# Kernel tuning notes

Measured on AMD Instinct MI355X. Metric: run time of the kernel, lower is better.

Reference implementation:

```python
import jax, jax.numpy as jnp
import numpy as np

MODEL_DIM = 1024
TOTAL_DIM = 1024
N_HEADS = 16
HEAD_DIM = TOTAL_DIM // N_HEADS


def setup_inputs() -> dict:
    key = jax.random.key(0)
    k1, k2, k3 = jax.random.split(key, 3)
    query = jax.random.normal(k1, (2, 2048, MODEL_DIM), dtype=jnp.float32)
    # nn.Linear(model_dim, 3*total_dim, bias=False): store as [in, out] for x @ W
    W_in = jax.random.normal(k2, (MODEL_DIM, 3 * TOTAL_DIM), dtype=jnp.float32) / np.sqrt(MODEL_DIM)
    W_out = jax.random.normal(k3, (TOTAL_DIM, MODEL_DIM), dtype=jnp.float32) / np.sqrt(TOTAL_DIM)
    return {"query": query, "W_in": W_in, "W_out": W_out}


def reference(query, W_in, W_out):
    B, S, _ = query.shape
    qkv = query @ W_in                      # [B, S, 3*D]
    q, k, v = jnp.split(qkv, 3, axis=-1)    # each [B, S, D]

    def to_heads(t):
        return t.reshape(B, S, N_HEADS, HEAD_DIM).transpose(0, 2, 1, 3)  # [B,H,S,d]

    q, k, v = to_heads(q), to_heads(k), to_heads(v)
    scale = 1.0 / np.sqrt(HEAD_DIM).astype(np.float32)
    scores = jnp.einsum('bhqd,bhkd->bhqk', q, k) * scale  # [B,H,S,S]
    causal = jnp.tril(jnp.ones((S, S), dtype=bool))
    scores = jnp.where(causal, scores, jnp.finfo(scores.dtype).min)
    probs = jax.nn.softmax(scores, axis=-1)
    attn = jnp.einsum('bhqk,bhkd->bhqd', probs, v)        # [B,H,S,d]
    attn = attn.transpose(0, 2, 1, 3).reshape(B, S, TOTAL_DIM)
    return attn @ W_out                     # [B, S, model_dim]
```

## Files before the change

### kernel.cpp

```cpp
#include <hip/hip_runtime.h>


typedef __bf16 bf16x8 __attribute__((ext_vector_type(8)));
typedef __bf16 bf16x4 __attribute__((ext_vector_type(4)));
typedef short s16x4 __attribute__((ext_vector_type(4)));
typedef float f32x4 __attribute__((ext_vector_type(4)));
typedef int i32x2 __attribute__((ext_vector_type(2)));

#define B_   2
#define S_   2048
#define DM   1024
#define NH   16
#define HD   64
#define N3   3072
#define M_   4096

#define SCALE_LOG2E 0.180336884f

__device__ __forceinline__ unsigned short f2bf(float f) {
  unsigned int u = __float_as_uint(f);
  u += 0x7fffu + ((u >> 16) & 1u);
  return (unsigned short)(u >> 16);
}

__device__ __forceinline__ void gload_lds16(void* lds, const void* g) {
  __builtin_amdgcn_global_load_lds(
      (__attribute__((address_space(1))) void*)g,
      (__attribute__((address_space(3))) void*)lds, 16, 0, 0);
}

__device__ __forceinline__ f32x4 mfma16(bf16x4 a, bf16x4 b, f32x4 c) {
#if __has_builtin(__builtin_amdgcn_mfma_f32_16x16x16_bf16)
  return __builtin_amdgcn_mfma_f32_16x16x16_bf16(a, b, c, 0, 0, 0);
#else
  return __builtin_amdgcn_mfma_f32_16x16x16bf16_1k(
      __builtin_bit_cast(s16x4, a), __builtin_bit_cast(s16x4, b), c, 0, 0, 0);
#endif
}

__device__ __forceinline__ int cvtpk(float s0, float s1) {
  int r;
  asm("v_cvt_pk_bf16_f32 %0, %1, %2" : "=v"(r) : "v"(s0), "v"(s1));
  return r;
}

__global__ __launch_bounds__(256) void prep(
    const float* __restrict__ query, const float* __restrict__ w_in,
    const float* __restrict__ w_out, unsigned short* __restrict__ qbf,
    unsigned short* __restrict__ w_in_t, unsigned short* __restrict__ w_out_t) {
  __shared__ float tile[32][33];
  const int bx = blockIdx.x;
  const int t = threadIdx.x;
  if (bx < 4096) {
    const int i = bx * 256 + t;
    const float4 v = ((const float4*)query)[i];
    ushort4 o;
    o.x = f2bf(v.x); o.y = f2bf(v.y); o.z = f2bf(v.z); o.w = f2bf(v.w);
    *(ushort4*)(&qbf[(size_t)i * 4]) = o;
    return;
  }
  const int tx = t & 31, ty = t >> 5;
  const float* in;
  unsigned short* out;
  int R, C, bxx, bxy, scale_rows;
  if (bx < 4096 + 3072) {
    const int id = bx - 4096;
    in = w_in; out = w_in_t; R = DM; C = N3;
    bxx = id % 96; bxy = id / 96; scale_rows = DM;
  } else {
    const int id = bx - 7168;
    in = w_out; out = w_out_t; R = DM; C = DM;
    bxx = id & 31; bxy = id >> 5; scale_rows = 0;
  }
  const int x = bxx * 32 + tx;
  const int y0 = bxy * 32;
#pragma unroll
  for (int j = 0; j < 32; j += 8)
    tile[ty + j][tx] = in[(size_t)(y0 + ty + j) * C + x];
  __syncthreads();
  const int ox = y0 + tx;
  const int oy0 = bxx * 32;
#pragma unroll
  for (int j = 0; j < 32; j += 8) {
    const int orow = oy0 + ty + j;
    float v = tile[tx][ty + j];
    if (orow < scale_rows) v *= SCALE_LOG2E;
    out[(size_t)orow * R + ox] = f2bf(v);
  }
}

__global__ __launch_bounds__(256) void gemm_qkv(
    const unsigned short* __restrict__ A, const unsigned short* __restrict__ Bt,
    unsigned short* __restrict__ qkv, unsigned short* __restrict__ vTn) {
  __shared__ __align__(16) unsigned short a_sm[128 * 32];
  __shared__ __align__(16) unsigned short b_sm[128 * 32];
  const int tid = threadIdx.x;
  const int lane = tid & 63, wave = tid >> 6;
  const int quad = lane >> 4, l15 = lane & 15;
  const int row0 = blockIdx.y * 128, col0 = blockIdx.x * 128;
  const int wm = (wave >> 1) * 64, wn = (wave & 1) * 64;
  const int K = DM;

  f32x4 acc[4][4];
#pragma unroll
  for (int i = 0; i < 4; i++)
#pragma unroll
    for (int j = 0; j < 4; j++) acc[i][j] = (f32x4){0.f, 0.f, 0.f, 0.f};

  const int e0 = tid * 8;

  for (int k0 = 0; k0 < K; k0 += 32) {
    __syncthreads();
#pragma unroll
    for (int i = 0; i < 2; i++) {
      int e = e0 + i * 2048;
      int r = e >> 5, c = e & 31;
      gload_lds16(&a_sm[e], &A[(size_t)(row0 + r) * K + k0 + c]);
      gload_lds16(&b_sm[e], &Bt[(size_t)(col0 + r) * K + k0 + c]);
    }
    __syncthreads();

    bf16x8 af[4], bfb[4];
#pragma unroll
    for (int i = 0; i < 4; i++) {
      af[i]  = *(const bf16x8*)&a_sm[(wm + i * 16 + l15) * 32 + quad * 8];
      bfb[i] = *(const bf16x8*)&b_sm[(wn + i * 16 + l15) * 32 + quad * 8];
    }
#pragma unroll
    for (int i = 0; i < 4; i++)
#pragma unroll
      for (int j = 0; j < 4; j++)
        acc[i][j] = __builtin_amdgcn_mfma_f32_16x16x32_bf16(af[i], bfb[j], acc[i][j], 0, 0, 0);
  }

  if (col0 + wn < 2 * DM) {
#pragma unroll
    for (int i = 0; i < 4; i++) {
#pragma unroll
      for (int j = 0; j < 4; j++) {
#pragma unroll
        for (int r = 0; r < 4; r++) {
          const int row = row0 + wm + i * 16 + quad * 4 + r;
          const int col = col0 + wn + j * 16 + l15;
          qkv[(size_t)row * N3 + col] = f2bf(acc[i][j][r]);
        }
      }
    }
  } else {
    const int head = (col0 + wn - 2 * DM) >> 6;
#pragma unroll
    for (int i = 0; i < 4; i++) {
      const int row = row0 + wm + i * 16 + quad * 4;
      const int b = row >> 11;
      const int srow = row & 2047;
      const int kt = srow >> 6;
      const int s = srow & 63;
      const int p = s >> 5, half = (s >> 4) & 1, q = (s >> 2) & 3;
      const size_t base = (size_t)((b * NH + head) * 32 + kt) * 4096;
#pragma unroll
      for (int j = 0; j < 4; j++) {
        const int d = j * 16 + l15;
        ushort4 w;
        w.x = f2bf(acc[i][j][0]);
        w.y = f2bf(acc[i][j][1]);
        w.z = f2bf(acc[i][j][2]);
        w.w = f2bf(acc[i][j][3]);
        *(ushort4*)&vTn[base + (size_t)(p * 256 + d * 4 + q) * 8 + half * 4] = w;
      }
    }
  }
}

__global__ __launch_bounds__(256) void gemm_abt_64(
    const unsigned short* __restrict__ A, const unsigned short* __restrict__ Bt,
    float* __restrict__ C, int M, int N, int K) {
  __shared__ __align__(16) unsigned short a_sm[64 * 32];
  __shared__ __align__(16) unsigned short b_sm[128 * 32];
  const int tid = threadIdx.x;
  const int lane = tid & 63, wave = tid >> 6;
  const int quad = lane >> 4, l15 = lane & 15;
  const int row0 = blockIdx.y * 64, col0 = blockIdx.x * 128;
  const int wn = wave * 32;

  f32x4 acc[4][2];
#pragma unroll
  for (int i = 0; i < 4; i++)
#pragma unroll
    for (int j = 0; j < 2; j++) acc[i][j] = (f32x4){0.f, 0.f, 0.f, 0.f};

  const int e0 = tid * 8;

  for (int k0 = 0; k0 < K; k0 += 32) {
    __syncthreads();
    {
      const int r = e0 >> 5, c = e0 & 31;
      gload_lds16(&a_sm[e0], &A[(size_t)(row0 + r) * K + k0 + c]);
    }
#pragma unroll
    for (int i = 0; i < 2; i++) {
      int e = e0 + i * 2048;
      int r = e >> 5, c = e & 31;
      gload_lds16(&b_sm[e], &Bt[(size_t)(col0 + r) * K + k0 + c]);
    }
    __syncthreads();

    bf16x8 af[4], bfb[2];
#pragma unroll
    for (int i = 0; i < 4; i++)
      af[i] = *(const bf16x8*)&a_sm[(i * 16 + l15) * 32 + quad * 8];
#pragma unroll
    for (int j = 0; j < 2; j++)
      bfb[j] = *(const bf16x8*)&b_sm[(wn + j * 16 + l15) * 32 + quad * 8];
#pragma unroll
    for (int i = 0; i < 4; i++)
#pragma unroll
      for (int j = 0; j < 2; j++)
        acc[i][j] = __builtin_amdgcn_mfma_f32_16x16x32_bf16(af[i], bfb[j], acc[i][j], 0, 0, 0);
  }

#pragma unroll
  for (int i = 0; i < 4; i++) {
#pragma unroll
    for (int j = 0; j < 2; j++) {
#pragma unroll
      for (int r = 0; r < 4; r++) {
        const int row = row0 + i * 16 + quad * 4 + r;
        const int col = col0 + wn + j * 16 + l15;
        C[(size_t)row * N + col] = acc[i][j][r];
      }
    }
  }
}

__global__ __launch_bounds__(512, 4) void attn_fused12(
    const unsigned short* __restrict__ qkv,
    const unsigned short* __restrict__ vTn,
    unsigned short* __restrict__ attnout) {
  const int h = blockIdx.y, b = blockIdx.z;
  const int j = blockIdx.x;
  const int tid = threadIdx.x;
  const int lane = tid & 63, wave = tid >> 6;
  const int quad = lane >> 4, l15 = lane & 15;
  const int sw = l15 & 7;

  __shared__ __align__(16) unsigned short k_sm[4 * 4096];
  __shared__ __align__(16) unsigned short vt_sm[4 * 4096];

  const int wrow0 = (wave < 4) ? (j * 64 + wave * 16)
                               : ((31 - j) * 64 + (wave - 4) * 16);
  const int qrow = wrow0 + l15;

  bf16x8 qf[2];
  {
    const unsigned short* qp = qkv + (size_t)(b * S_ + qrow) * N3 + h * HD + quad * 8;
    qf[0] = *(const bf16x8*)qp;
    qf[1] = *(const bf16x8*)(qp + 32);
  }

  f32x4 o[4];
#pragma unroll
  for (int n = 0; n < 4; n++) o[n] = (f32x4){0.f, 0.f, 0.f, 0.f};
  float lsum = 0.f;

  const int r0s = tid >> 3;
  const int gch = ((tid & 7) ^ (r0s & 7)) * 8;
  const unsigned short* kgb = qkv + (size_t)(b * S_ + r0s) * N3 + DM + h * HD + gch;
  const unsigned short* vgl = vTn + (size_t)((b * NH + h) * 32) * 4096 + tid * 8;

  const int nt = 32 - j;

  int pk[4][2];
  const unsigned short* vbp = &vt_sm[0];

  auto PV = [&]() {
    __builtin_amdgcn_s_setprio(1);
#pragma unroll
    for (int p = 0; p < 2; p++) {
      i32x2 wlo, whi;
      wlo.x = pk[2 * p][0];     wlo.y = pk[2 * p][1];
      whi.x = pk[2 * p + 1][0]; whi.y = pk[2 * p + 1][1];
      const bf16x4 blo = __builtin_bit_cast(bf16x4, wlo);
      const bf16x4 bhi = __builtin_bit_cast(bf16x4, whi);
#pragma unroll
      for (int mb = 0; mb < 4; mb++) {
        const bf16x8 vv =
            *(const bf16x8*)&vbp[(p * 256 + mb * 64 + l15 * 4 + quad) * 8];
        bf16x4 alo, ahi;
#pragma unroll
        for (int i = 0; i < 4; i++) { alo[i] = vv[i]; ahi[i] = vv[i + 4]; }
        o[mb] = mfma16(alo, blo, o[mb]);
        o[mb] = mfma16(ahi, bhi, o[mb]);
      }
    }
    __builtin_amdgcn_s_setprio(0);
  };

  gload_lds16(&k_sm[tid * 8], kgb);
  gload_lds16(&vt_sm[tid * 8], vgl);
  gload_lds16(&k_sm[4096 + tid * 8], kgb + (size_t)64 * N3);
  gload_lds16(&vt_sm[4096 + tid * 8], vgl + 4096);

  for (int t = 0; t < nt; t++) {
    if (t + 1 < nt) asm volatile("s_waitcnt vmcnt(2)" ::: "memory");
    else            asm volatile("s_waitcnt vmcnt(0)" ::: "memory");
    __builtin_amdgcn_s_barrier();
    __builtin_amdgcn_sched_barrier(0);
    if (t + 2 < nt) {
      const int b2 = (t + 2) & 3;
      gload_lds16(&k_sm[b2 * 4096 + tid * 8], kgb + (size_t)(t + 2) * 64 * N3);
      gload_lds16(&vt_sm[b2 * 4096 + tid * 8], vgl + (size_t)(t + 2) * 4096);
    }
    const unsigned short* kb = &k_sm[(t & 3) * 4096];
    const unsigned short* vb = &vt_sm[(t & 3) * 4096];

    if (t >= 1 && (t - 1) * 64 <= wrow0 + 15) PV();

    if (t * 64 <= wrow0 + 15) {
      f32x4 s[4];
#pragma unroll
      for (int mb = 0; mb < 4; mb++) s[mb] = (f32x4){0.f, 0.f, 0.f, 0.f};
      __builtin_amdgcn_s_setprio(1);
#pragma unroll
      for (int mb = 0; mb < 4; mb++) {
        const int ro = (mb * 16 + l15) * 64;
        bf16x8 kf0 = *(const bf16x8*)&kb[ro + ((quad ^ sw) << 3)];
        bf16x8 kf1 = *(const bf16x8*)&kb[ro + (((4 + quad) ^ sw) << 3)];
        s[mb] = __builtin_amdgcn_mfma_f32_16x16x32_bf16(kf0, qf[0], s[mb], 0, 0, 0);
        s[mb] = __builtin_amdgcn_mfma_f32_16x16x32_bf16(kf1, qf[1], s[mb], 0, 0, 0);
      }
      __builtin_amdgcn_s_setprio(0);

      if (t * 64 + 63 <= wrow0) {
#pragma unroll
        for (int mb = 0; mb < 4; mb++)
#pragma unroll
          for (int r = 0; r < 4; r++)
            s[mb][r] = exp2f(s[mb][r]);
      } else {
        const int kq0 = t * 64 + quad * 4;
#pragma unroll
        for (int mb = 0; mb < 4; mb++)
#pragma unroll
          for (int r = 0; r < 4; r++) {
            const float e = exp2f(s[mb][r]);
            s[mb][r] = (kq0 + mb * 16 + r <= qrow) ? e : 0.f;
          }
      }
#pragma unroll
      for (int mb = 0; mb < 4; mb++)
        lsum += (s[mb][0] + s[mb][1]) + (s[mb][2] + s[mb][3]);

#pragma unroll
      for (int mb = 0; mb < 4; mb++) {
        pk[mb][0] = cvtpk(s[mb][0], s[mb][1]);
        pk[mb][1] = cvtpk(s[mb][2], s[mb][3]);
      }
      vbp = vb;
    }
  }

  if ((nt - 1) * 64 <= wrow0 + 15) PV();

  asm volatile("s_waitcnt vmcnt(0)" ::: "memory");

  float l = lsum;
  l += __shfl_xor(l, 16);
  l += __shfl_xor(l, 32);
  const float inv = 1.0f / l;
  const size_t grow = (size_t)(b * S_ + qrow);
#pragma unroll
  for (int mb = 0; mb < 4; mb++) {
    ushort4 w;
    w.x = f2bf(o[mb][0] * inv);
    w.y = f2bf(o[mb][1] * inv);
    w.z = f2bf(o[mb][2] * inv);
    w.w = f2bf(o[mb][3] * inv);
    *(ushort4*)&attnout[grow * DM + h * HD + mb * 16 + quad * 4] = w;
  }
}

extern "C" void kernel_launch(void* const* d_in, const int* in_sizes, int n_in,
                              void* d_out, int out_size, void* d_ws, size_t ws_size,
                              hipStream_t stream) {
  const float* query = (const float*)d_in[0];
  const float* w_in  = (const float*)d_in[1];
  const float* w_out = (const float*)d_in[2];
  float* out = (float*)d_out;

  char* ws = (char*)d_ws;
  unsigned short* qbf     = (unsigned short*)(ws);
  unsigned short* attn    = (unsigned short*)(ws);
  unsigned short* w_in_t  = (unsigned short*)(ws + 8388608);
  unsigned short* w_out_t = (unsigned short*)(ws + 14680064);
  unsigned short* qkv     = (unsigned short*)(ws + 16777216);
  unsigned short* vTn     = (unsigned short*)(ws + 41943040);

  prep<<<dim3(8192), dim3(256), 0, stream>>>(query, w_in, w_out, qbf, w_in_t, w_out_t);
  gemm_qkv<<<dim3(N3 / 128, M_ / 128), dim3(256), 0, stream>>>(qbf, w_in_t, qkv, vTn);
  attn_fused12<<<dim3(16, NH, B_), dim3(512), 0, stream>>>(qkv, vTn, attn);
  gemm_abt_64<<<dim3(DM / 128, M_ / 64), dim3(256), 0, stream>>>(attn, w_out_t, out, M_, DM, DM);
}
```

Baseline: 192.7 us.

## Process KV tiles in pairs per barrier and remap blocks for XCD locality

The attention loop now handles two 64-key tiles per barrier round, with one vmcnt(0) wait, instead of one barrier per tile. Each tile's QK^T, exp and PV run back to back in the same step, replacing the previous software pipeline that delayed PV by one iteration. Block indices are also permuted so that consecutive hardware block IDs, which are round-robined across 8 XCDs, map to nearby (b,h) work and so share L2. The cost is less overlap between global loads and compute, since the kernel waits on all outstanding loads each round, and PV now sits right behind the exp dependency.

```diff
diff --git a/kernel.cpp b/kernel.cpp
--- a/kernel.cpp
+++ b/kernel.cpp
@@ -232,12 +232,16 @@
   }
 }
 
-__global__ __launch_bounds__(512, 4) void attn_fused12(
+__global__ __launch_bounds__(512, 4) void attn_fused13(
     const unsigned short* __restrict__ qkv,
     const unsigned short* __restrict__ vTn,
     unsigned short* __restrict__ attnout) {
-  const int h = blockIdx.y, b = blockIdx.z;
-  const int j = blockIdx.x;
+  const int p = blockIdx.x + (blockIdx.y << 4) + (blockIdx.z << 8);
+  const int lg = ((p & 7) << 6) + (p >> 3);
+  const int j = lg & 15;
+  const int h = (lg >> 4) & 15;
+  const int b = lg >> 8;
+
   const int tid = threadIdx.x;
   const int lane = tid & 63, wave = tid >> 6;
   const int quad = lane >> 4, l15 = lane & 15;
@@ -268,23 +272,71 @@
   const unsigned short* vgl = vTn + (size_t)((b * NH + h) * 32) * 4096 + tid * 8;
 
   const int nt = 32 - j;
-
-  int pk[4][2];
-  const unsigned short* vbp = &vt_sm[0];
-
-  auto PV = [&]() {
+  const int nR = (nt + 1) >> 1;
+
+  auto STAGE = [&](int t) {
+    const int bu = (t & 3) * 4096;
+    gload_lds16(&k_sm[bu + tid * 8], kgb + (size_t)t * 64 * N3);
+    gload_lds16(&vt_sm[bu + tid * 8], vgl + (size_t)t * 4096);
+  };
+
+  auto SUBTILE = [&](int t) {
+    const unsigned short* kb = &k_sm[(t & 3) * 4096];
+    const unsigned short* vb = &vt_sm[(t & 3) * 4096];
+
+    f32x4 s[4];
+#pragma unroll
+    for (int mb = 0; mb < 4; mb++) s[mb] = (f32x4){0.f, 0.f, 0.f, 0.f};
     __builtin_amdgcn_s_setprio(1);
 #pragma unroll
-    for (int p = 0; p < 2; p++) {
+    for (int mb = 0; mb < 4; mb++) {
+      const int ro = (mb * 16 + l15) * 64;
+      bf16x8 kf0 = *(const bf16x8*)&kb[ro + ((quad ^ sw) << 3)];
+      bf16x8 kf1 = *(const bf16x8*)&kb[ro + (((4 + quad) ^ sw) << 3)];
+      s[mb] = __builtin_amdgcn_mfma_f32_16x16x32_bf16(kf0, qf[0], s[mb], 0, 0, 0);
+      s[mb] = __builtin_amdgcn_mfma_f32_16x16x32_bf16(kf1, qf[1], s[mb], 0, 0, 0);
+    }
+    __builtin_amdgcn_s_setprio(0);
+
+    if (t * 64 + 63 <= wrow0) {
+#pragma unroll
+      for (int mb = 0; mb < 4; mb++)
+#pragma unroll
+        for (int r = 0; r < 4; r++)
+          s[mb][r] = exp2f(s[mb][r]);
+    } else {
+      const int kq0 = t * 64 + quad * 4;
+#pragma unroll
+      for (int mb = 0; mb < 4; mb++)
+#pragma unroll
+        for (int r = 0; r < 4; r++) {
+          const float e = exp2f(s[mb][r]);
+          s[mb][r] = (kq0 + mb * 16 + r <= qrow) ? e : 0.f;
+        }
+    }
+#pragma unroll
+    for (int mb = 0; mb < 4; mb++)
+      lsum += (s[mb][0] + s[mb][1]) + (s[mb][2] + s[mb][3]);
+
+    int pk[4][2];
+#pragma unroll
+    for (int mb = 0; mb < 4; mb++) {
+      pk[mb][0] = cvtpk(s[mb][0], s[mb][1]);
+      pk[mb][1] = cvtpk(s[mb][2], s[mb][3]);
+    }
+
+    __builtin_amdgcn_s_setprio(1);
+#pragma unroll
+    for (int pp = 0; pp < 2; pp++) {
       i32x2 wlo, whi;
-      wlo.x = pk[2 * p][0];     wlo.y = pk[2 * p][1];
-      whi.x = pk[2 * p + 1][0]; whi.y = pk[2 * p + 1][1];
+      wlo.x = pk[2 * pp][0];     wlo.y = pk[2 * pp][1];
+      whi.x = pk[2 * pp + 1][0]; whi.y = pk[2 * pp + 1][1];
       const bf16x4 blo = __builtin_bit_cast(bf16x4, wlo);
       const bf16x4 bhi = __builtin_bit_cast(bf16x4, whi);
 #pragma unroll
       for (int mb = 0; mb < 4; mb++) {
         const bf16x8 vv =
-            *(const bf16x8*)&vbp[(p * 256 + mb * 64 + l15 * 4 + quad) * 8];
+            *(const bf16x8*)&vb[(pp * 256 + mb * 64 + l15 * 4 + quad) * 8];
         bf16x4 alo, ahi;
 #pragma unroll
         for (int i = 0; i < 4; i++) { alo[i] = vv[i]; ahi[i] = vv[i + 4]; }
@@ -295,71 +347,21 @@
     __builtin_amdgcn_s_setprio(0);
   };
 
-  gload_lds16(&k_sm[tid * 8], kgb);
-  gload_lds16(&vt_sm[tid * 8], vgl);
-  gload_lds16(&k_sm[4096 + tid * 8], kgb + (size_t)64 * N3);
-  gload_lds16(&vt_sm[4096 + tid * 8], vgl + 4096);
-
-  for (int t = 0; t < nt; t++) {
-    if (t + 1 < nt) asm volatile("s_waitcnt vmcnt(2)" ::: "memory");
-    else            asm volatile("s_waitcnt vmcnt(0)" ::: "memory");
+  STAGE(0);
+  if (1 < nt) STAGE(1);
+
+  for (int r = 0; r < nR; r++) {
+    const int t0 = 2 * r, t1 = 2 * r + 1;
+    asm volatile("s_waitcnt vmcnt(0)" ::: "memory");
     __builtin_amdgcn_s_barrier();
     __builtin_amdgcn_sched_barrier(0);
-    if (t + 2 < nt) {
-      const int b2 = (t + 2) & 3;
-      gload_lds16(&k_sm[b2 * 4096 + tid * 8], kgb + (size_t)(t + 2) * 64 * N3);
-      gload_lds16(&vt_sm[b2 * 4096 + tid * 8], vgl + (size_t)(t + 2) * 4096);
-    }
-    const unsigned short* kb = &k_sm[(t & 3) * 4096];
-    const unsigned short* vb = &vt_sm[(t & 3) * 4096];
-
-    if (t >= 1 && (t - 1) * 64 <= wrow0 + 15) PV();
-
-    if (t * 64 <= wrow0 + 15) {
-      f32x4 s[4];
-#pragma unroll
-      for (int mb = 0; mb < 4; mb++) s[mb] = (f32x4){0.f, 0.f, 0.f, 0.f};
-      __builtin_amdgcn_s_setprio(1);
-#pragma unroll
-      for (int mb = 0; mb < 4; mb++) {
-        const int ro = (mb * 16 + l15) * 64;
-        bf16x8 kf0 = *(const bf16x8*)&kb[ro + ((quad ^ sw) << 3)];
-        bf16x8 kf1 = *(const bf16x8*)&kb[ro + (((4 + quad) ^ sw) << 3)];
-        s[mb] = __builtin_amdgcn_mfma_f32_16x16x32_bf16(kf0, qf[0], s[mb], 0, 0, 0);
-        s[mb] = __builtin_amdgcn_mfma_f32_16x16x32_bf16(kf1, qf[1], s[mb], 0, 0, 0);
-      }
-      __builtin_amdgcn_s_setprio(0);
-
-      if (t * 64 + 63 <= wrow0) {
-#pragma unroll
-        for (int mb = 0; mb < 4; mb++)
-#pragma unroll
-          for (int r = 0; r < 4; r++)
-            s[mb][r] = exp2f(s[mb][r]);
-      } else {
-        const int kq0 = t * 64 + quad * 4;
-#pragma unroll
-        for (int mb = 0; mb < 4; mb++)
-#pragma unroll
-          for (int r = 0; r < 4; r++) {
-            const float e = exp2f(s[mb][r]);
-            s[mb][r] = (kq0 + mb * 16 + r <= qrow) ? e : 0.f;
-          }
-      }
-#pragma unroll
-      for (int mb = 0; mb < 4; mb++)
-        lsum += (s[mb][0] + s[mb][1]) + (s[mb][2] + s[mb][3]);
-
-#pragma unroll
-      for (int mb = 0; mb < 4; mb++) {
-        pk[mb][0] = cvtpk(s[mb][0], s[mb][1]);
-        pk[mb][1] = cvtpk(s[mb][2], s[mb][3]);
-      }
-      vbp = vb;
-    }
-  }
-
-  if ((nt - 1) * 64 <= wrow0 + 15) PV();
+    if (r + 1 < nR) {
+      STAGE(t0 + 2);
+      if (t1 + 2 < nt) STAGE(t1 + 2);
+    }
+    if (t0 * 64 <= wrow0 + 15) SUBTILE(t0);
+    if (t1 < nt && t1 * 64 <= wrow0 + 15) SUBTILE(t1);
+  }
 
   asm volatile("s_waitcnt vmcnt(0)" ::: "memory");
 
@@ -397,6 +399,6 @@
 
   prep<<<dim3(8192), dim3(256), 0, stream>>>(query, w_in, w_out, qbf, w_in_t, w_out_t);
   gemm_qkv<<<dim3(N3 / 128, M_ / 128), dim3(256), 0, stream>>>(qbf, w_in_t, qkv, vTn);
-  attn_fused12<<<dim3(16, NH, B_), dim3(512), 0, stream>>>(qkv, vTn, attn);
+  attn_fused13<<<dim3(16, NH, B_), dim3(512), 0, stream>>>(qkv, vTn, attn);
   gemm_abt_64<<<dim3(DM / 128, M_ / 64), dim3(256), 0, stream>>>(attn, w_out_t, out, M_, DM, DM);
 }
```

Result: no change. 189.4 us (-1.7%).
